# Optimization experiments

Hardware: AMD Instinct MI355X
Metric: run time of the kernel (lower is better)

Reference implementation:

```python
import jax, jax.numpy as jnp
import numpy as np

N, E, D = 50000, 400000, 64
L, NA, NS = 5, 4, 3            # layers, num aggregators, num scalers
ATOM_C, ATOM_V = 9, 64         # OGB-style atom feature columns / vocab
BOND_C, BOND_V = 3, 8
EPS = 1e-5
AVG_LOG = float(np.log(9.0))   # avg_d['log'] = ln(avg_degree + 1), avg_degree = 8


def setup_inputs() -> dict:
    key = jax.random.key(0)
    ks = jax.random.split(key, 8)
    x = jax.random.randint(ks[0], (N, ATOM_C), 0, ATOM_V)
    edge_index = jax.random.randint(ks[1], (2, E), 0, N)
    edge_attr = jax.random.randint(ks[2], (E, BOND_C), 0, BOND_V)
    init = lambda k, shape, fan: (jax.random.normal(k, shape, jnp.float32) / np.sqrt(fan))
    atom_emb = init(ks[3], (ATOM_C, ATOM_V, D), D)
    bond_emb = init(ks[4], (BOND_C, BOND_V, D), D)
    pre_W = init(ks[5], (L, 3 * D, D), 3 * D)                 # pretrans: Linear(3D -> D)
    pre_b = jnp.zeros((L, D), jnp.float32)
    post_W = init(ks[6], (L, (NA * NS + 1) * D, D), (NA * NS + 1) * D)  # posttrans: Linear(13D -> D)
    post_b = jnp.zeros((L, D), jnp.float32)
    return dict(x=x, edge_index=edge_index, edge_attr=edge_attr,
                atom_emb=atom_emb, bond_emb=bond_emb,
                pre_W=pre_W, pre_b=pre_b, post_W=post_W, post_b=post_b)


def reference(x, edge_index, edge_attr, atom_emb, bond_emb, pre_W, pre_b, post_W, post_b):
    src, dst = edge_index[0], edge_index[1]  # PyG: x_j = x[edge_index[0]], x_i = x[edge_index[1]]
    # Encoders: sum of per-column categorical embeddings (OGB Atom/BondEncoder)
    h0 = atom_emb[jnp.arange(ATOM_C)[None, :], x].sum(axis=1)        # [N, D]
    e = bond_emb[jnp.arange(BOND_C)[None, :], edge_attr].sum(axis=1)  # [E, D]
    # message input cat([x_i, x_j, edge_attr]) -- identical for every layer since
    # PNAGNN.forward never feeds layer output back in as x (faithful to source)
    z2 = jnp.concatenate([h0[dst], h0[src], e], axis=-1)              # [E, 3D]
    deg = jax.ops.segment_sum(jnp.ones((E,), jnp.float32), dst, num_segments=N)
    degc = jnp.maximum(deg, 1.0)[:, None]
    log_deg = jnp.log(jnp.maximum(deg, 1.0) + 1.0)[:, None]           # guard deg=0 for attenuation
    amp = log_deg / AVG_LOG
    att = AVG_LOG / log_deg
    has = (deg > 0)[:, None]
    h_in = h0
    for l in range(L):
        m = z2 @ pre_W[l] + pre_b[l]                                  # pretrans (1 layer, no act)
        s_sum = jax.ops.segment_sum(m, dst, num_segments=N)
        mean = s_sum / degc
        mx = jnp.where(has, jax.ops.segment_max(m, dst, num_segments=N), 0.0)
        mn = jnp.where(has, jax.ops.segment_min(m, dst, num_segments=N), 0.0)
        mean_sq = jax.ops.segment_sum(m * m, dst, num_segments=N) / degc
        var = jax.nn.relu(mean_sq - mean * mean)
        std = jnp.sqrt(var + EPS)
        agg = jnp.concatenate([mean, mx, mn, std], axis=-1)           # [N, 4D]
        scaled = jnp.concatenate([agg, agg * amp, agg * att], axis=-1)  # [N, 12D]
        hcat = jnp.concatenate([scaled, h0], axis=-1)                 # [N, 13D]
        out = hcat @ post_W[l] + post_b[l]                            # posttrans (1 layer, no act)
        h = out + h_in                                                # PNAGNN residual
        h_in = h
    return h
```

## Files before the change

### kernel.cpp

```cpp
#include <hip/hip_runtime.h>
#include <hip/hip_bf16.h>

#define NN 50000
#define NE 400000
#define AVG_LOG_F 2.1972245773362196f
#define EPSV 1e-5f

typedef __hip_bfloat16 bf16;
typedef __attribute__((ext_vector_type(8))) short short8v;
typedef __attribute__((ext_vector_type(4))) float f32x4;

__device__ __forceinline__ float b2f(bf16 v){ return __bfloat162float(v); }
__device__ __forceinline__ bf16  f2b(float v){ return __float2bfloat16(v); }
__device__ __forceinline__ short f2s(float v){
  bf16 b = __float2bfloat16(v);
  short s; __builtin_memcpy(&s, &b, 2); return s;
}
__device__ __forceinline__ float s2f(short v){
  bf16 b; __builtin_memcpy(&b, &v, 2); return __bfloat162float(b);
}

__global__ void k_h0(const int* __restrict__ x, const float* __restrict__ aemb,
                     bf16* __restrict__ h0b){
  int idx = blockIdx.x * 256 + threadIdx.x;
  if (idx >= NN * 64) return;
  int n = idx >> 6, d = idx & 63;
  float acc = 0.f;
  #pragma unroll
  for (int c = 0; c < 9; ++c){
    int a = x[n * 9 + c];
    acc += aemb[(c * 64 + a) * 64 + d];
  }
  h0b[idx] = f2b(acc);
}

__global__ void k_deg_code(const int* __restrict__ ei, const int* __restrict__ ea,
                           int* __restrict__ deg, int* __restrict__ code){
  int e = blockIdx.x * 256 + threadIdx.x;
  if (e >= NE) return;
  int dst = ei[NE + e];
  atomicAdd(&deg[dst], 1);
  code[e] = ea[e * 3] + 8 * ea[e * 3 + 1] + 64 * ea[e * 3 + 2];
}

__global__ void k_scan1(const int* __restrict__ deg, int* __restrict__ rowptr,
                        int* __restrict__ part){
  __shared__ int s[256];
  int t = threadIdx.x, i = blockIdx.x * 256 + t;
  int v = (i < NN) ? deg[i] : 0;
  s[t] = v; __syncthreads();
  for (int off = 1; off < 256; off <<= 1){
    int xv = (t >= off) ? s[t - off] : 0;
    __syncthreads();
    s[t] += xv;
    __syncthreads();
  }
  if (i < NN) rowptr[i] = s[t] - v;
  if (t == 255) part[blockIdx.x] = s[255];
}

__global__ void k_scan2(int* __restrict__ part, int nblk){
  __shared__ int s[256];
  int t = threadIdx.x;
  int v = (t < nblk) ? part[t] : 0;
  s[t] = v; __syncthreads();
  for (int off = 1; off < 256; off <<= 1){
    int xv = (t >= off) ? s[t - off] : 0;
    __syncthreads();
    s[t] += xv;
    __syncthreads();
  }
  if (t < nblk) part[t] = s[t] - v;
}

__global__ void k_scan3(int* __restrict__ rowptr, const int* __restrict__ part,
                        const int* __restrict__ deg, float* __restrict__ amp,
                        float* __restrict__ att){
  int i = blockIdx.x * 256 + threadIdx.x;
  if (i < NN){
    rowptr[i] += part[blockIdx.x];
    int d = deg[i];
    float ld = logf((float)max(d, 1) + 1.0f);
    amp[i] = ld / AVG_LOG_F;
    att[i] = AVG_LOG_F / ld;
  }
  if (i == 0) rowptr[NN] = NE;
}

__global__ void k_scatter(const int* __restrict__ ei, const int* __restrict__ code,
                          const int* __restrict__ rowptr, int* __restrict__ cursor,
                          int2* __restrict__ sedge){
  int e = blockIdx.x * 256 + threadIdx.x;
  if (e >= NE) return;
  int dst = ei[NE + e];
  int pos = rowptr[dst] + atomicAdd(&cursor[dst], 1);
  int2 v; v.x = ei[e]; v.y = code[e];
  sedge[pos] = v;
}

__global__ void k_ctab(const float* __restrict__ bemb, const float* __restrict__ preW,
                       bf16* __restrict__ CTp){
  __shared__ float et[64];
  int cb = blockIdx.x, l = blockIdx.y, t = threadIdx.x;
  int a0 = cb & 7, a1 = (cb >> 3) & 7, a2 = (cb >> 6) & 7;
  et[t] = bemb[(0 * 8 + a0) * 64 + t] + bemb[(1 * 8 + a1) * 64 + t] + bemb[(2 * 8 + a2) * 64 + t];
  __syncthreads();
  float acc = 0.f;
  const float* W = preW + (l * 192 + 128) * 64;
  for (int k = 0; k < 64; ++k) acc += et[k] * W[k * 64 + t];
  CTp[((size_t)cb * 64 + t) * 8 + l] = f2b(acc);
}

__global__ void k_whsum(const float* __restrict__ postW, const float* __restrict__ postb,
                        float* __restrict__ whs, float* __restrict__ bs){
  int idx = blockIdx.x * 256 + threadIdx.x;
  if (idx < 4096){
    int k = idx >> 6, d = idx & 63;
    float a = 0.f;
    for (int l = 0; l < 5; ++l) a += postW[(size_t)(l * 832 + 768 + k) * 64 + d];
    whs[idx] = a;
  }
  if (idx < 64){
    float a = 0.f;
    for (int l = 0; l < 5; ++l) a += postb[l * 64 + idx];
    bs[idx] = a;
  }
}

__global__ void k_wtk(const float* __restrict__ postW, bf16* __restrict__ WtK){
  int idx = blockIdx.x * 256 + threadIdx.x;
  if (idx >= 3 * 64 * 1280) return;
  int g = idx / (64 * 1280);
  int rem = idx % (64 * 1280);
  int c = rem / 1280;
  int kk = rem % 1280;
  int l = kk >> 8, k = kk & 255;
  WtK[idx] = f2b(postW[((size_t)l * 832 + g * 256 + k) * 64 + c]);
}

__global__ void k_wtpre896(const float* __restrict__ preW, const float* __restrict__ preb,
                           const float* __restrict__ whs, const float* __restrict__ bs,
                           bf16* __restrict__ Wtp, float* __restrict__ bias896){
  int idx = blockIdx.x * 256 + threadIdx.x;
  if (idx < 896 * 64){
    int gc = idx >> 6, k = idx & 63;
    float v;
    if (gc < 320){
      int l = gc >> 6, c = gc & 63;
      v = preW[(size_t)(l * 192 + k) * 64 + c];
    } else if (gc < 832){
      int q = gc - 320, d = q >> 3, l = q & 7;
      v = (l < 5) ? preW[(size_t)(l * 192 + 64 + k) * 64 + d] : 0.f;
    } else {
      int c = gc - 832;
      v = whs[k * 64 + c] + ((k == c) ? 1.f : 0.f);
    }
    Wtp[idx] = f2b(v);
  }
  if (idx < 896){
    float b;
    if (idx < 320)      b = preb[(idx >> 6) * 64 + (idx & 63)];
    else if (idx < 832) b = 0.f;
    else                b = bs[idx - 832];
    bias896[idx] = b;
  }
}

__global__ __launch_bounds__(256) void k_ab_mfma(const bf16* __restrict__ h0b,
                                                 const bf16* __restrict__ Wtp,
                                                 const float* __restrict__ bias896,
                                                 bf16* __restrict__ ABU,
                                                 float* __restrict__ out){
  __shared__ bf16 As[128][72];
  __shared__ bf16 Bs[128][72];
  const int t = threadIdx.x;
  const int n0 = blockIdx.x * 128;
  const int gc0 = blockIdx.y * 128;
  const int lane = t & 63, wid = t >> 6;
  const int rw = wid * 32;
  const short* H  = (const short*)h0b;
  const short* Wp = (const short*)Wtp;

  #pragma unroll
  for (int i = 0; i < 4; ++i){
    int idx = t + i * 256;
    int r = idx >> 3, ko = (idx & 7) * 8;
    int n = n0 + r;
    short8v v = short8v{0,0,0,0,0,0,0,0};
    if (n < NN) v = *(const short8v*)(H + (size_t)n * 64 + ko);
    *(short8v*)&As[r][ko] = v;
  }
  #pragma unroll
  for (int i = 0; i < 4; ++i){
    int idx = t + i * 256;
    int cc = idx >> 3, ko = (idx & 7) * 8;
    *(short8v*)&Bs[cc][ko] = *(const short8v*)(Wp + (size_t)(gc0 + cc) * 64 + ko);
  }
  __syncthreads();

  f32x4 acc[2][8] = {};
  #pragma unroll
  for (int kk = 0; kk < 2; ++kk){
    short8v af0 = *(const short8v*)&As[rw + (lane & 15)][kk * 32 + (lane >> 4) * 8];
    short8v af1 = *(const short8v*)&As[rw + 16 + (lane & 15)][kk * 32 + (lane >> 4) * 8];
    #pragma unroll
    for (int j = 0; j < 8; ++j){
      short8v bfj = *(const short8v*)&Bs[j * 16 + (lane & 15)][kk * 32 + (lane >> 4) * 8];
      acc[0][j] = __builtin_amdgcn_mfma_f32_16x16x32_bf16(af0, bfj, acc[0][j], 0, 0, 0);
      acc[1][j] = __builtin_amdgcn_mfma_f32_16x16x32_bf16(af1, bfj, acc[1][j], 0, 0, 0);
    }
  }

  #pragma unroll
  for (int i = 0; i < 2; ++i){
    #pragma unroll
    for (int r = 0; r < 4; ++r){
      int n = n0 + rw + i * 16 + (lane >> 4) * 4 + r;
      if (n >= NN) continue;
      #pragma unroll
      for (int j = 0; j < 8; ++j){
        int gc = gc0 + j * 16 + (lane & 15);
        float v = acc[i][j][r] + bias896[gc];
        if (gc < 832) ABU[(size_t)n * 832 + gc] = f2b(v);
        else          out[(size_t)n * 64 + (gc - 832)] = v;
      }
    }
  }
}

__global__ __launch_bounds__(512) void k_gather(const bf16* __restrict__ ABU,
                                                const bf16* __restrict__ CTp,
                                                const int* __restrict__ rowptr,
                                                const int2* __restrict__ sedge,
                                                bf16* __restrict__ AGG){
  const int t = threadIdx.x, lane = t & 63, wid = t >> 6;
  const int n = blockIdx.x * 8 + wid;
  const short* ABUs = (const short*)ABU;
  const short* CTps = (const short*)CTp;
  short* AGs = (short*)AGG;

  int r0 = rowptr[n], r1 = rowptr[n + 1];
  float s[5]  = {0.f, 0.f, 0.f, 0.f, 0.f};
  float sq[5] = {0.f, 0.f, 0.f, 0.f, 0.f};
  float mx[5], mn[5];
  #pragma unroll
  for (int l = 0; l < 5; ++l){ mx[l] = -1e30f; mn[l] = 1e30f; }

  for (int j = r0; j < r1; j += 4){
    int rem = r1 - j;
    int2 e0 = sedge[j];
    int2 e1 = (rem > 1) ? sedge[j + 1] : e0;
    int2 e2 = (rem > 2) ? sedge[j + 2] : e0;
    int2 e3 = (rem > 3) ? sedge[j + 3] : e0;
    short8v a0 = *(const short8v*)(ABUs + (size_t)e0.x * 832 + 320 + lane * 8);
    short8v c0 = *(const short8v*)(CTps + (size_t)e0.y * 512 + lane * 8);
    short8v a1 = *(const short8v*)(ABUs + (size_t)e1.x * 832 + 320 + lane * 8);
    short8v c1 = *(const short8v*)(CTps + (size_t)e1.y * 512 + lane * 8);
    short8v a2 = *(const short8v*)(ABUs + (size_t)e2.x * 832 + 320 + lane * 8);
    short8v c2 = *(const short8v*)(CTps + (size_t)e2.y * 512 + lane * 8);
    short8v a3 = *(const short8v*)(ABUs + (size_t)e3.x * 832 + 320 + lane * 8);
    short8v c3 = *(const short8v*)(CTps + (size_t)e3.y * 512 + lane * 8);

    #pragma unroll
    for (int l = 0; l < 5; ++l){
      float tv = s2f(a0[l]) + s2f(c0[l]);
      s[l] += tv; sq[l] = fmaf(tv, tv, sq[l]);
      mx[l] = fmaxf(mx[l], tv); mn[l] = fminf(mn[l], tv);
    }
    if (rem > 1){
      #pragma unroll
      for (int l = 0; l < 5; ++l){
        float tv = s2f(a1[l]) + s2f(c1[l]);
        s[l] += tv; sq[l] = fmaf(tv, tv, sq[l]);
        mx[l] = fmaxf(mx[l], tv); mn[l] = fminf(mn[l], tv);
      }
    }
    if (rem > 2){
      #pragma unroll
      for (int l = 0; l < 5; ++l){
        float tv = s2f(a2[l]) + s2f(c2[l]);
        s[l] += tv; sq[l] = fmaf(tv, tv, sq[l]);
        mx[l] = fmaxf(mx[l], tv); mn[l] = fminf(mn[l], tv);
      }
    }
    if (rem > 3){
      #pragma unroll
      for (int l = 0; l < 5; ++l){
        float tv = s2f(a3[l]) + s2f(c3[l]);
        s[l] += tv; sq[l] = fmaf(tv, tv, sq[l]);
        mx[l] = fmaxf(mx[l], tv); mn[l] = fminf(mn[l], tv);
      }
    }
  }

  int d = r1 - r0;
  float degc = (float)((d > 0) ? d : 1);
  size_t base = (size_t)n * 1280;
  #pragma unroll
  for (int l = 0; l < 5; ++l){
    float K = s2f(ABUs[(size_t)n * 832 + l * 64 + lane]);
    float mean = ((float)d * K + s[l]) / degc;
    float MX = (d > 0) ? (K + mx[l]) : 0.f;
    float MN = (d > 0) ? (K + mn[l]) : 0.f;
    float mu = s[l] / degc;
    float var = fmaxf(sq[l] / degc - mu * mu, 0.f);
    float sd = sqrtf(var + EPSV);
    AGs[base + l * 256 + lane]       = f2s(mean);
    AGs[base + l * 256 + 64 + lane]  = f2s(MX);
    AGs[base + l * 256 + 128 + lane] = f2s(MN);
    AGs[base + l * 256 + 192 + lane] = f2s(sd);
  }
}

__global__ __launch_bounds__(256) void k_post5(const bf16* __restrict__ AGG,
                                               const bf16* __restrict__ WtK,
                                               const float* __restrict__ amp,
                                               const float* __restrict__ att,
                                               float* __restrict__ out){
  __shared__ short As[64][136];
  const int t = threadIdx.x, lane = t & 63, wid = t >> 6;
  const int n0 = blockIdx.x * 64;
  const short* AGs = (const short*)AGG;
  const short* Ws  = (const short*)WtK;

  f32x4 acc[4][3] = {};
  for (int kt = 0; kt < 10; ++kt){
    __syncthreads();
    #pragma unroll
    for (int i = 0; i < 4; ++i){
      int id = t + i * 256;
      int r = id >> 4, ko = (id & 15) * 8;
      int n = n0 + r;
      short8v v = short8v{0,0,0,0,0,0,0,0};
      if (n < NN) v = *(const short8v*)(AGs + (size_t)n * 1280 + kt * 128 + ko);
      *(short8v*)&As[r][ko] = v;
    }
    __syncthreads();
    #pragma unroll
    for (int kk = 0; kk < 4; ++kk){
      short8v bfg[3];
      #pragma unroll
      for (int g = 0; g < 3; ++g)
        bfg[g] = *(const short8v*)(Ws + (size_t)(g * 64 + wid * 16 + (lane & 15)) * 1280 +
                                   kt * 128 + kk * 32 + (lane >> 4) * 8);
      #pragma unroll
      for (int rf = 0; rf < 4; ++rf){
        short8v af = *(const short8v*)&As[rf * 16 + (lane & 15)][kk * 32 + (lane >> 4) * 8];
        #pragma unroll
        for (int g = 0; g < 3; ++g)
          acc[rf][g] = __builtin_amdgcn_mfma_f32_16x16x32_bf16(af, bfg[g], acc[rf][g], 0, 0, 0);
      }
    }
  }

  #pragma unroll
  for (int rf = 0; rf < 4; ++rf){
    #pragma unroll
    for (int r = 0; r < 4; ++r){
      int n = n0 + rf * 16 + (lane >> 4) * 4 + r;
      if (n >= NN) continue;
      float am = amp[n], at = att[n];
      int c = wid * 16 + (lane & 15);
      out[(size_t)n * 64 + c] += acc[rf][0][r] + am * acc[rf][1][r] + at * acc[rf][2][r];
    }
  }
}

extern "C" void kernel_launch(void* const* d_in, const int* in_sizes, int n_in,
                              void* d_out, int out_size, void* d_ws, size_t ws_size,
                              hipStream_t stream){
  const int*   x     = (const int*)d_in[0];
  const int*   ei    = (const int*)d_in[1];
  const int*   ea    = (const int*)d_in[2];
  const float* aemb  = (const float*)d_in[3];
  const float* bemb  = (const float*)d_in[4];
  const float* preW  = (const float*)d_in[5];
  const float* preb  = (const float*)d_in[6];
  const float* postW = (const float*)d_in[7];
  const float* postb = (const float*)d_in[8];
  float* out = (float*)d_out;

  char* p = (char*)d_ws;
  auto alloc = [&](size_t bytes) -> char* {
    char* r = p;
    p += (bytes + 255) & ~(size_t)255;
    return r;
  };
  bf16*  h0b     = (bf16*) alloc((size_t)NN * 64 * 2);
  bf16*  ABU     = (bf16*) alloc((size_t)NN * 832 * 2);
  bf16*  AGG     = (bf16*) alloc((size_t)NN * 1280 * 2);
  int*   deg     = (int*)  alloc((size_t)NN * 4);
  int*   rowptr  = (int*)  alloc((size_t)(NN + 1) * 4);
  int*   cursor  = (int*)  alloc((size_t)NN * 4);
  float* amp     = (float*)alloc((size_t)NN * 4);
  float* att     = (float*)alloc((size_t)NN * 4);
  int*   code    = (int*)  alloc((size_t)NE * 4);
  int2*  sedge   = (int2*) alloc((size_t)NE * 8);
  bf16*  CTp     = (bf16*) alloc((size_t)512 * 64 * 8 * 2);
  float* whs     = (float*)alloc((size_t)64 * 64 * 4);
  float* bs      = (float*)alloc((size_t)64 * 4);
  int*   part    = (int*)  alloc((size_t)256 * 4);
  bf16*  WtK     = (bf16*) alloc((size_t)3 * 64 * 1280 * 2);
  bf16*  Wtp     = (bf16*) alloc((size_t)896 * 64 * 2);
  float* bias896 = (float*)alloc((size_t)896 * 4);
  if ((size_t)(p - (char*)d_ws) > ws_size) return;

  hipMemsetAsync(deg, 0, (size_t)NN * 4, stream);
  hipMemsetAsync(cursor, 0, (size_t)NN * 4, stream);

  k_h0<<<dim3((NN * 64 + 255) / 256), 256, 0, stream>>>(x, aemb, h0b);
  k_deg_code<<<dim3((NE + 255) / 256), 256, 0, stream>>>(ei, ea, deg, code);
  int nblk = (NN + 255) / 256;
  k_scan1<<<dim3(nblk), 256, 0, stream>>>(deg, rowptr, part);
  k_scan2<<<dim3(1), 256, 0, stream>>>(part, nblk);
  k_scan3<<<dim3(nblk), 256, 0, stream>>>(rowptr, part, deg, amp, att);
  k_scatter<<<dim3((NE + 255) / 256), 256, 0, stream>>>(ei, code, rowptr, cursor, sedge);
  k_ctab<<<dim3(512, 5), 64, 0, stream>>>(bemb, preW, CTp);
  k_whsum<<<dim3(16), 256, 0, stream>>>(postW, postb, whs, bs);
  k_wtk<<<dim3((3 * 64 * 1280 + 255) / 256), 256, 0, stream>>>(postW, WtK);
  k_wtpre896<<<dim3((896 * 64 + 255) / 256), 256, 0, stream>>>(preW, preb, whs, bs,
                                                               Wtp, bias896);
  k_ab_mfma<<<dim3((NN + 127) / 128, 7), 256, 0, stream>>>(h0b, Wtp, bias896, ABU, out);
  k_gather<<<dim3(NN / 8), 512, 0, stream>>>(ABU, CTp, rowptr, sedge, AGG);
  k_post5<<<dim3((NN + 63) / 64), 256, 0, stream>>>(AGG, WtK, amp, att, out);
}
```

Before: 288.2 us.

## Use fp16 packed max/min in gather, resize gather blocks, double-buffer post GEMM

Intermediate ABU and edge table are stored in fp16 instead of bf16, so the gather kernel can run max/min with packed half2 ops and avoid some scalar conversions. The gather kernel moves from 512-thread to 256-thread blocks. The post-transform GEMM now handles 128 rows per 512-thread block and double-buffers the shared-memory A tiles, prefetching the next K slice into registers while the MFMAs run. fp16 trades exponent range for mantissa precision, so large intermediate values could overflow.

```diff
diff --git a/kernel.cpp b/kernel.cpp
--- a/kernel.cpp
+++ b/kernel.cpp
@@ -9,6 +9,7 @@
 typedef __hip_bfloat16 bf16;
 typedef __attribute__((ext_vector_type(8))) short short8v;
 typedef __attribute__((ext_vector_type(4))) float f32x4;
+typedef __attribute__((ext_vector_type(2))) _Float16 h2v;
 
 __device__ __forceinline__ float b2f(bf16 v){ return __bfloat162float(v); }
 __device__ __forceinline__ bf16  f2b(float v){ return __float2bfloat16(v); }
@@ -99,7 +100,7 @@
 }
 
 __global__ void k_ctab(const float* __restrict__ bemb, const float* __restrict__ preW,
-                       bf16* __restrict__ CTp){
+                       _Float16* __restrict__ CTp){
   __shared__ float et[64];
   int cb = blockIdx.x, l = blockIdx.y, t = threadIdx.x;
   int a0 = cb & 7, a1 = (cb >> 3) & 7, a2 = (cb >> 6) & 7;
@@ -108,7 +109,7 @@
   float acc = 0.f;
   const float* W = preW + (l * 192 + 128) * 64;
   for (int k = 0; k < 64; ++k) acc += et[k] * W[k * 64 + t];
-  CTp[((size_t)cb * 64 + t) * 8 + l] = f2b(acc);
+  CTp[((size_t)cb * 64 + t) * 8 + l] = (_Float16)acc;
 }
 
 __global__ void k_whsum(const float* __restrict__ postW, const float* __restrict__ postb,
@@ -169,7 +170,7 @@
 __global__ __launch_bounds__(256) void k_ab_mfma(const bf16* __restrict__ h0b,
                                                  const bf16* __restrict__ Wtp,
                                                  const float* __restrict__ bias896,
-                                                 bf16* __restrict__ ABU,
+                                                 _Float16* __restrict__ ABU,
                                                  float* __restrict__ out){
   __shared__ bf16 As[128][72];
   __shared__ bf16 Bs[128][72];
@@ -221,20 +222,20 @@
       for (int j = 0; j < 8; ++j){
         int gc = gc0 + j * 16 + (lane & 15);
         float v = acc[i][j][r] + bias896[gc];
-        if (gc < 832) ABU[(size_t)n * 832 + gc] = f2b(v);
+        if (gc < 832) ABU[(size_t)n * 832 + gc] = (_Float16)v;
         else          out[(size_t)n * 64 + (gc - 832)] = v;
       }
     }
   }
 }
 
-__global__ __launch_bounds__(512) void k_gather(const bf16* __restrict__ ABU,
-                                                const bf16* __restrict__ CTp,
+__global__ __launch_bounds__(256) void k_gather(const _Float16* __restrict__ ABU,
+                                                const _Float16* __restrict__ CTp,
                                                 const int* __restrict__ rowptr,
                                                 const int2* __restrict__ sedge,
                                                 bf16* __restrict__ AGG){
   const int t = threadIdx.x, lane = t & 63, wid = t >> 6;
-  const int n = blockIdx.x * 8 + wid;
+  const int n = blockIdx.x * 4 + wid;
   const short* ABUs = (const short*)ABU;
   const short* CTps = (const short*)CTp;
   short* AGs = (short*)AGG;
@@ -242,9 +243,12 @@
   int r0 = rowptr[n], r1 = rowptr[n + 1];
   float s[5]  = {0.f, 0.f, 0.f, 0.f, 0.f};
   float sq[5] = {0.f, 0.f, 0.f, 0.f, 0.f};
-  float mx[5], mn[5];
-  #pragma unroll
-  for (int l = 0; l < 5; ++l){ mx[l] = -1e30f; mn[l] = 1e30f; }
+  const _Float16 FLO = (_Float16)(-65504.f);
+  const _Float16 FHI = (_Float16)( 65504.f);
+  h2v mx01 = h2v{FLO, FLO}, mx23 = h2v{FLO, FLO}, mx45 = h2v{FLO, FLO};
+  h2v mn01 = h2v{FHI, FHI}, mn23 = h2v{FHI, FHI}, mn45 = h2v{FHI, FHI};
+
+  union P8 { short8v s; h2v h[4]; };
 
   for (int j = r0; j < r1; j += 4){
     int rem = r1 - j;
@@ -252,53 +256,51 @@
     int2 e1 = (rem > 1) ? sedge[j + 1] : e0;
     int2 e2 = (rem > 2) ? sedge[j + 2] : e0;
     int2 e3 = (rem > 3) ? sedge[j + 3] : e0;
-    short8v a0 = *(const short8v*)(ABUs + (size_t)e0.x * 832 + 320 + lane * 8);
-    short8v c0 = *(const short8v*)(CTps + (size_t)e0.y * 512 + lane * 8);
-    short8v a1 = *(const short8v*)(ABUs + (size_t)e1.x * 832 + 320 + lane * 8);
-    short8v c1 = *(const short8v*)(CTps + (size_t)e1.y * 512 + lane * 8);
-    short8v a2 = *(const short8v*)(ABUs + (size_t)e2.x * 832 + 320 + lane * 8);
-    short8v c2 = *(const short8v*)(CTps + (size_t)e2.y * 512 + lane * 8);
-    short8v a3 = *(const short8v*)(ABUs + (size_t)e3.x * 832 + 320 + lane * 8);
-    short8v c3 = *(const short8v*)(CTps + (size_t)e3.y * 512 + lane * 8);
-
-    #pragma unroll
-    for (int l = 0; l < 5; ++l){
-      float tv = s2f(a0[l]) + s2f(c0[l]);
-      s[l] += tv; sq[l] = fmaf(tv, tv, sq[l]);
-      mx[l] = fmaxf(mx[l], tv); mn[l] = fminf(mn[l], tv);
-    }
-    if (rem > 1){
-      #pragma unroll
-      for (int l = 0; l < 5; ++l){
-        float tv = s2f(a1[l]) + s2f(c1[l]);
-        s[l] += tv; sq[l] = fmaf(tv, tv, sq[l]);
-        mx[l] = fmaxf(mx[l], tv); mn[l] = fminf(mn[l], tv);
-      }
-    }
-    if (rem > 2){
-      #pragma unroll
-      for (int l = 0; l < 5; ++l){
-        float tv = s2f(a2[l]) + s2f(c2[l]);
-        s[l] += tv; sq[l] = fmaf(tv, tv, sq[l]);
-        mx[l] = fmaxf(mx[l], tv); mn[l] = fminf(mn[l], tv);
-      }
-    }
-    if (rem > 3){
-      #pragma unroll
-      for (int l = 0; l < 5; ++l){
-        float tv = s2f(a3[l]) + s2f(c3[l]);
-        s[l] += tv; sq[l] = fmaf(tv, tv, sq[l]);
-        mx[l] = fmaxf(mx[l], tv); mn[l] = fminf(mn[l], tv);
-      }
-    }
-  }
+    P8 a0, c0, a1, c1, a2, c2, a3, c3;
+    a0.s = *(const short8v*)(ABUs + (size_t)e0.x * 832 + 320 + lane * 8);
+    c0.s = *(const short8v*)(CTps + (size_t)e0.y * 512 + lane * 8);
+    a1.s = *(const short8v*)(ABUs + (size_t)e1.x * 832 + 320 + lane * 8);
+    c1.s = *(const short8v*)(CTps + (size_t)e1.y * 512 + lane * 8);
+    a2.s = *(const short8v*)(ABUs + (size_t)e2.x * 832 + 320 + lane * 8);
+    c2.s = *(const short8v*)(CTps + (size_t)e2.y * 512 + lane * 8);
+    a3.s = *(const short8v*)(ABUs + (size_t)e3.x * 832 + 320 + lane * 8);
+    c3.s = *(const short8v*)(CTps + (size_t)e3.y * 512 + lane * 8);
+
+    #define EDGE_ACC(A, C) {                                        \
+      h2v t01 = A.h[0] + C.h[0];                                    \
+      h2v t23 = A.h[1] + C.h[1];                                    \
+      h2v t45 = A.h[2] + C.h[2];                                    \
+      mx01 = __builtin_elementwise_max(mx01, t01);                  \
+      mx23 = __builtin_elementwise_max(mx23, t23);                  \
+      mx45 = __builtin_elementwise_max(mx45, t45);                  \
+      mn01 = __builtin_elementwise_min(mn01, t01);                  \
+      mn23 = __builtin_elementwise_min(mn23, t23);                  \
+      mn45 = __builtin_elementwise_min(mn45, t45);                  \
+      float f0 = (float)t01[0], f1 = (float)t01[1];                 \
+      float f2 = (float)t23[0], f3 = (float)t23[1];                 \
+      float f4 = (float)t45[0];                                     \
+      s[0] += f0; sq[0] = fmaf(f0, f0, sq[0]);                      \
+      s[1] += f1; sq[1] = fmaf(f1, f1, sq[1]);                      \
+      s[2] += f2; sq[2] = fmaf(f2, f2, sq[2]);                      \
+      s[3] += f3; sq[3] = fmaf(f3, f3, sq[3]);                      \
+      s[4] += f4; sq[4] = fmaf(f4, f4, sq[4]);                      \
+    }
+    EDGE_ACC(a0, c0);
+    if (rem > 1) EDGE_ACC(a1, c1);
+    if (rem > 2) EDGE_ACC(a2, c2);
+    if (rem > 3) EDGE_ACC(a3, c3);
+    #undef EDGE_ACC
+  }
+
+  float mx[5] = {(float)mx01[0], (float)mx01[1], (float)mx23[0], (float)mx23[1], (float)mx45[0]};
+  float mn[5] = {(float)mn01[0], (float)mn01[1], (float)mn23[0], (float)mn23[1], (float)mn45[0]};
 
   int d = r1 - r0;
   float degc = (float)((d > 0) ? d : 1);
   size_t base = (size_t)n * 1280;
   #pragma unroll
   for (int l = 0; l < 5; ++l){
-    float K = s2f(ABUs[(size_t)n * 832 + l * 64 + lane]);
+    float K = (float)ABU[(size_t)n * 832 + l * 64 + lane];
     float mean = ((float)d * K + s[l]) / degc;
     float MX = (d > 0) ? (K + mx[l]) : 0.f;
     float MN = (d > 0) ? (K + mn[l]) : 0.f;
@@ -312,55 +314,79 @@
   }
 }
 
-__global__ __launch_bounds__(256) void k_post5(const bf16* __restrict__ AGG,
+__global__ __launch_bounds__(512) void k_post5(const bf16* __restrict__ AGG,
                                                const bf16* __restrict__ WtK,
                                                const float* __restrict__ amp,
                                                const float* __restrict__ att,
                                                float* __restrict__ out){
-  __shared__ short As[64][136];
+  __shared__ short As[2][128][140];
   const int t = threadIdx.x, lane = t & 63, wid = t >> 6;
-  const int n0 = blockIdx.x * 64;
+  const int n0 = blockIdx.x * 128;
+  const int w4 = wid & 3, rh = wid >> 2;
   const short* AGs = (const short*)AGG;
   const short* Ws  = (const short*)WtK;
+  const short8v zv = short8v{0,0,0,0,0,0,0,0};
+
+  #pragma unroll
+  for (int i = 0; i < 4; ++i){
+    int id = t + i * 512;
+    int r = id >> 4, ko = (id & 15) * 8;
+    int n = n0 + r;
+    short8v v = zv;
+    if (n < NN) v = *(const short8v*)(AGs + (size_t)n * 1280 + ko);
+    *(short8v*)&As[0][r][ko] = v;
+  }
+  __syncthreads();
 
   f32x4 acc[4][3] = {};
   for (int kt = 0; kt < 10; ++kt){
-    __syncthreads();
-    #pragma unroll
-    for (int i = 0; i < 4; ++i){
-      int id = t + i * 256;
-      int r = id >> 4, ko = (id & 15) * 8;
-      int n = n0 + r;
-      short8v v = short8v{0,0,0,0,0,0,0,0};
-      if (n < NN) v = *(const short8v*)(AGs + (size_t)n * 1280 + kt * 128 + ko);
-      *(short8v*)&As[r][ko] = v;
-    }
-    __syncthreads();
+    const int cur = kt & 1;
+    short8v pref[4];
+    if (kt < 9){
+      #pragma unroll
+      for (int i = 0; i < 4; ++i){
+        int id = t + i * 512;
+        int r = id >> 4, ko = (id & 15) * 8;
+        int n = n0 + r;
+        pref[i] = zv;
+        if (n < NN) pref[i] = *(const short8v*)(AGs + (size_t)n * 1280 + (kt + 1) * 128 + ko);
+      }
+    }
     #pragma unroll
     for (int kk = 0; kk < 4; ++kk){
       short8v bfg[3];
       #pragma unroll
       for (int g = 0; g < 3; ++g)
-        bfg[g] = *(const short8v*)(Ws + (size_t)(g * 64 + wid * 16 + (lane & 15)) * 1280 +
+        bfg[g] = *(const short8v*)(Ws + (size_t)(g * 64 + w4 * 16 + (lane & 15)) * 1280 +
                                    kt * 128 + kk * 32 + (lane >> 4) * 8);
       #pragma unroll
       for (int rf = 0; rf < 4; ++rf){
-        short8v af = *(const short8v*)&As[rf * 16 + (lane & 15)][kk * 32 + (lane >> 4) * 8];
+        short8v af = *(const short8v*)&As[cur][rh * 64 + rf * 16 + (lane & 15)]
+                                         [kk * 32 + (lane >> 4) * 8];
         #pragma unroll
         for (int g = 0; g < 3; ++g)
           acc[rf][g] = __builtin_amdgcn_mfma_f32_16x16x32_bf16(af, bfg[g], acc[rf][g], 0, 0, 0);
       }
     }
+    if (kt < 9){
+      #pragma unroll
+      for (int i = 0; i < 4; ++i){
+        int id = t + i * 512;
+        int r = id >> 4, ko = (id & 15) * 8;
+        *(short8v*)&As[cur ^ 1][r][ko] = pref[i];
+      }
+    }
+    __syncthreads();
   }
 
   #pragma unroll
   for (int rf = 0; rf < 4; ++rf){
     #pragma unroll
     for (int r = 0; r < 4; ++r){
-      int n = n0 + rf * 16 + (lane >> 4) * 4 + r;
+      int n = n0 + rh * 64 + rf * 16 + (lane >> 4) * 4 + r;
       if (n >= NN) continue;
       float am = amp[n], at = att[n];
-      int c = wid * 16 + (lane & 15);
+      int c = w4 * 16 + (lane & 15);
       out[(size_t)n * 64 + c] += acc[rf][0][r] + am * acc[rf][1][r] + at * acc[rf][2][r];
     }
   }
@@ -386,23 +412,23 @@
     p += (bytes + 255) & ~(size_t)255;
     return r;
   };
-  bf16*  h0b     = (bf16*) alloc((size_t)NN * 64 * 2);
-  bf16*  ABU     = (bf16*) alloc((size_t)NN * 832 * 2);
-  bf16*  AGG     = (bf16*) alloc((size_t)NN * 1280 * 2);
-  int*   deg     = (int*)  alloc((size_t)NN * 4);
-  int*   rowptr  = (int*)  alloc((size_t)(NN + 1) * 4);
-  int*   cursor  = (int*)  alloc((size_t)NN * 4);
-  float* amp     = (float*)alloc((size_t)NN * 4);
-  float* att     = (float*)alloc((size_t)NN * 4);
-  int*   code    = (int*)  alloc((size_t)NE * 4);
-  int2*  sedge   = (int2*) alloc((size_t)NE * 8);
-  bf16*  CTp     = (bf16*) alloc((size_t)512 * 64 * 8 * 2);
-  float* whs     = (float*)alloc((size_t)64 * 64 * 4);
-  float* bs      = (float*)alloc((size_t)64 * 4);
-  int*   part    = (int*)  alloc((size_t)256 * 4);
-  bf16*  WtK     = (bf16*) alloc((size_t)3 * 64 * 1280 * 2);
-  bf16*  Wtp     = (bf16*) alloc((size_t)896 * 64 * 2);
-  float* bias896 = (float*)alloc((size_t)896 * 4);
+  bf16*      h0b     = (bf16*)     alloc((size_t)NN * 64 * 2);
+  _Float16*  ABU     = (_Float16*) alloc((size_t)NN * 832 * 2);
+  bf16*      AGG     = (bf16*)     alloc((size_t)NN * 1280 * 2);
+  int*       deg     = (int*)      alloc((size_t)NN * 4);
+  int*       rowptr  = (int*)      alloc((size_t)(NN + 1) * 4);
+  int*       cursor  = (int*)      alloc((size_t)NN * 4);
+  float*     amp     = (float*)    alloc((size_t)NN * 4);
+  float*     att     = (float*)    alloc((size_t)NN * 4);
+  int*       code    = (int*)      alloc((size_t)NE * 4);
+  int2*      sedge   = (int2*)     alloc((size_t)NE * 8);
+  _Float16*  CTp     = (_Float16*) alloc((size_t)512 * 64 * 8 * 2 + 64);
+  float*     whs     = (float*)    alloc((size_t)64 * 64 * 4);
+  float*     bs      = (float*)    alloc((size_t)64 * 4);
+  int*       part    = (int*)      alloc((size_t)256 * 4);
+  bf16*      WtK     = (bf16*)     alloc((size_t)3 * 64 * 1280 * 2);
+  bf16*      Wtp     = (bf16*)     alloc((size_t)896 * 64 * 2);
+  float*     bias896 = (float*)    alloc((size_t)896 * 4);
   if ((size_t)(p - (char*)d_ws) > ws_size) return;
 
   hipMemsetAsync(deg, 0, (size_t)NN * 4, stream);
@@ -421,6 +447,6 @@
   k_wtpre896<<<dim3((896 * 64 + 255) / 256), 256, 0, stream>>>(preW, preb, whs, bs,
                                                                Wtp, bias896);
   k_ab_mfma<<<dim3((NN + 127) / 128, 7), 256, 0, stream>>>(h0b, Wtp, bias896, ABU, out);
-  k_gather<<<dim3(NN / 8), 512, 0, stream>>>(ABU, CTp, rowptr, sedge, AGG);
-  k_post5<<<dim3((NN + 63) / 64), 256, 0, stream>>>(AGG, WtK, amp, att, out);
-}
+  k_gather<<<dim3(NN / 4), 256, 0, stream>>>(ABU, CTp, rowptr, sedge, AGG);
+  k_post5<<<dim3((NN + 127) / 128), 512, 0, stream>>>(AGG, WtK, amp, att, out);
+}
```

Measured after the change: 290.5 us. About the same (+0.8%).
